# Performance work log

Measured on AMD Instinct MI355X. Metric: run time of the kernel, lower is better.

Reference implementation:

```python
import jax, jax.numpy as jnp
import numpy as np

N = 1024   # nodes
E = 65536  # edges per relation
H = 2      # attention heads
NEG_SLOPE = 0.2


def _add_self_loops(ei, n):
    loop = jnp.arange(n, dtype=ei.dtype)
    return jnp.concatenate([ei, jnp.stack([loop, loop])], axis=1)


def _gat(x, ei, W, a_src, a_dst, bias, n):
    # PyG GATConv (heads=H, concat=True): project, edge attention, segment softmax, scatter-sum
    h, c = a_src.shape
    xp = (x @ W).reshape(n, h, c)                      # [n, H, C]
    src, dst = ei[0], ei[1]
    al_s = jnp.einsum('nhc,hc->nh', xp, a_src)         # [n, H]
    al_d = jnp.einsum('nhc,hc->nh', xp, a_dst)
    alpha = jax.nn.leaky_relu(al_s[src] + al_d[dst], NEG_SLOPE)  # [E, H]
    m = jax.ops.segment_max(alpha, dst, num_segments=n)
    m = jnp.where(jnp.isfinite(m), m, 0.0)
    m = jax.lax.stop_gradient(m)
    e = jnp.exp(alpha - m[dst])
    s = jax.ops.segment_sum(e, dst, num_segments=n)
    a = e / (s[dst] + 1e-16)                           # segment softmax over incoming edges
    out = jax.ops.segment_sum(xp[src] * a[:, :, None], dst, num_segments=n)
    return out.reshape(n, h * c) + bias


def setup_inputs():
    key = jax.random.key(0)
    ks = jax.random.split(key, 32)
    d = {}
    d['x'] = jax.random.normal(ks[0], (N, 256), dtype=jnp.float32)
    d['ei0'] = jax.random.randint(ks[1], (2, E), 0, N)
    d['ei1'] = jax.random.randint(ks[2], (2, E), 0, N)
    k = 3
    # layer 1: in 256 -> H*256 = 512 per relation
    for r in range(2):
        d[f'W1_{r}'] = jax.random.normal(ks[k], (256, H * 256), jnp.float32) * 0.0625; k += 1
        d[f'as1_{r}'] = jax.random.normal(ks[k], (H, 256), jnp.float32) * 0.0625; k += 1
        d[f'ad1_{r}'] = jax.random.normal(ks[k], (H, 256), jnp.float32) * 0.0625; k += 1
        d[f'b1_{r}'] = jnp.zeros((H * 256,), jnp.float32)
    # layer 2: in 512 -> H*64 = 128 per relation
    for r in range(2):
        d[f'W2_{r}'] = jax.random.normal(ks[k], (512, H * 64), jnp.float32) * 0.0442; k += 1
        d[f'as2_{r}'] = jax.random.normal(ks[k], (H, 64), jnp.float32) * 0.125; k += 1
        d[f'ad2_{r}'] = jax.random.normal(ks[k], (H, 64), jnp.float32) * 0.125; k += 1
        d[f'b2_{r}'] = jnp.zeros((H * 64,), jnp.float32)
    d['w_lin'] = jax.random.normal(ks[k], (H * 64, 1), jnp.float32) * 0.088; k += 1
    d['b_lin'] = jnp.zeros((1,), jnp.float32)
    return d


def reference(x, ei0, ei1, W1_0, as1_0, ad1_0, b1_0, W1_1, as1_1, ad1_1, b1_1,
              W2_0, as2_0, ad2_0, b2_0, W2_1, as2_1, ad2_1, b2_1, w_lin, b_lin):
    e0 = _add_self_loops(ei0, N)
    e1 = _add_self_loops(ei1, N)
    # HeteroConv aggr='sum' over the two relations
    h1 = _gat(x, e0, W1_0, as1_0, ad1_0, b1_0, N) + _gat(x, e1, W1_1, as1_1, ad1_1, b1_1, N)
    h1 = jax.nn.relu(h1)
    h2 = _gat(h1, e0, W2_0, as2_0, ad2_0, b2_0, N) + _gat(h1, e1, W2_1, as2_1, ad2_1, b2_1, N)
    # dense pairwise sum over all node pairs: [N*N, 128]
    pairs = (h2[:, None, :] + h2[None, :, :]).reshape(N * N, h2.shape[-1])
    return pairs @ w_lin + b_lin
```

## Files before the change

### kernel.cpp

```cpp
#include <hip/hip_runtime.h>
#include <hip/hip_bf16.h>


#define NEG_SLOPE 0.2f
static __device__ __forceinline__ float lrelu(float x){ return x > 0.f ? x : NEG_SLOPE * x; }

#define NN 1024
#define SLOTS 192

static __device__ __forceinline__ int norm_cnt(int raw){
    return raw < -1000000000 ? raw - (int)0xAAAAAAAAu : raw;
}

struct P {
    const float *x; const int *ei0, *ei1;
    const float *W1_0,*as1_0,*ad1_0,*b1_0, *W1_1,*as1_1,*ad1_1,*b1_1;
    const float *W2_0,*as2_0,*ad2_0,*b2_0, *W2_1,*as2_1,*ad2_1,*b2_1;
    const float *wlin, *blin;
    float *out;
    __hip_bfloat162 *xp1_0,*xp1_1;
    float *L1;
    float *wc;
    float *nb;
    float *q, *qb;
    int *cnt;
    int *eb0,*eb1;
    int E;
};

__global__ __launch_bounds__(256)
void k1_scatter_gemm1(P p){
    __shared__ float As[32][68];
    __shared__ float Bs[32][68];
    const int b = blockIdx.x, t = threadIdx.x;

    if (b < 128){
        const int TOT = p.E + NN;
        for (int i = b*256 + t; i < 2*TOT; i += 128*256){
            int r = i >= TOT, e = i - r*TOT;
            const int* ei = r ? p.ei1 : p.ei0;
            int src, dst;
            if (e < p.E){ src = ei[e]; dst = ei[p.E + e]; } else { src = dst = e - p.E; }
            int pos = norm_cnt(atomicAdd(&p.cnt[r*NN + dst], 1));
            if (pos >= 0 && pos < SLOTS) (r ? p.eb1 : p.eb0)[dst*SLOTS + pos] = src;
        }
        return;
    }
    if (b >= 384){
        int idx2 = b - 384;
        int r = idx2 >> 2, k0 = (idx2 & 3) * 128;
        const float* W2 = r ? p.W2_1 : p.W2_0;
        const float* as2 = r ? p.as2_1 : p.as2_0;
        const float* ad2 = r ? p.ad2_1 : p.ad2_0;
        if (t < 128){
            int k = k0 + t;
            float sa[2] = {0.f,0.f}, da[2] = {0.f,0.f}, za[2] = {0.f,0.f};
            #pragma unroll
            for (int h = 0; h < 2; h++){
                for (int c = 0; c < 64; c++){
                    float w = W2[k*128 + h*64 + c];
                    sa[h] += w * as2[h*64 + c];
                    da[h] += w * ad2[h*64 + c];
                    za[h] += w * p.wlin[h*64 + c];
                }
            }
            float* wcr = p.wc + r*6*512;
            wcr[0*512 + k] = sa[0]; wcr[1*512 + k] = sa[1];
            wcr[2*512 + k] = da[0]; wcr[3*512 + k] = da[1];
            wcr[4*512 + k] = za[0]; wcr[5*512 + k] = za[1];
        }
        if (b == 384 && t == 128){
            float s = 0.f;
            for (int k = 0; k < 128; k++) s += (p.b2_0[k] + p.b2_1[k]) * p.wlin[k];
            p.qb[0] = s;
        }
        return;
    }
    int idx = b - 128;
    int r = idx >> 7, t2 = idx & 127;
    int m0 = (t2 >> 3) * 64, n0 = (t2 & 7) * 64;
    const float* B = r ? p.W1_1 : p.W1_0;
    __hip_bfloat162* C = r ? p.xp1_1 : p.xp1_0;
    int tx = t & 15, ty = t >> 4;
    float acc[4][4] = {};
    for (int k0 = 0; k0 < 256; k0 += 32){
        float4 a4[2], b4[2];
        #pragma unroll
        for (int u = 0; u < 2; u++){
            int f = u*256 + t;
            int am = f >> 3, ac4 = f & 7;
            a4[u] = *(const float4*)(p.x + (size_t)(m0+am)*256 + k0 + ac4*4);
            int bk = f >> 4, bc4 = f & 15;
            b4[u] = *(const float4*)(B + (size_t)(k0+bk)*512 + n0 + bc4*4);
        }
        __syncthreads();
        #pragma unroll
        for (int u = 0; u < 2; u++){
            int f = u*256 + t;
            int am = f >> 3, ac4 = f & 7;
            As[ac4*4+0][am] = a4[u].x; As[ac4*4+1][am] = a4[u].y;
            As[ac4*4+2][am] = a4[u].z; As[ac4*4+3][am] = a4[u].w;
            int bk = f >> 4, bc4 = f & 15;
            *(float4*)&Bs[bk][bc4*4] = b4[u];
        }
        __syncthreads();
        #pragma unroll
        for (int kk = 0; kk < 32; kk++){
            float4 av = *(const float4*)&As[kk][ty*4];
            float4 bv = *(const float4*)&Bs[kk][tx*4];
            float ar[4] = {av.x, av.y, av.z, av.w};
            float br[4] = {bv.x, bv.y, bv.z, bv.w};
            #pragma unroll
            for (int i = 0; i < 4; i++)
                #pragma unroll
                for (int j = 0; j < 4; j++)
                    acc[i][j] += ar[i] * br[j];
        }
        __syncthreads();
    }
    #pragma unroll
    for (int i = 0; i < 4; i++){
        int row = m0 + ty*4 + i, col = n0 + tx*4;
        __hip_bfloat162 t0, t1;
        t0.x = __float2bfloat16(acc[i][0]); t0.y = __float2bfloat16(acc[i][1]);
        t1.x = __float2bfloat16(acc[i][2]); t1.y = __float2bfloat16(acc[i][3]);
        size_t o2 = ((size_t)row*512 + col) >> 1;
        C[o2] = t0; C[o2 + 1] = t1;
    }
    {
        int h = n0 >> 8;
        const float* as_ = r ? p.as1_1 : p.as1_0;
        const float* ad_ = r ? p.ad1_1 : p.ad1_0;
        float a_s[4], a_d[4];
        #pragma unroll
        for (int u = 0; u < 4; u++){
            a_s[u] = as_[n0 + tx*4 + u];
            a_d[u] = ad_[n0 + tx*4 + u];
        }
        #pragma unroll
        for (int i = 0; i < 4; i++){
            float ps = acc[i][0]*a_s[0] + acc[i][1]*a_s[1]
                     + acc[i][2]*a_s[2] + acc[i][3]*a_s[3];
            float pd = acc[i][0]*a_d[0] + acc[i][1]*a_d[1]
                     + acc[i][2]*a_d[2] + acc[i][3]*a_d[3];
            #pragma unroll
            for (int o = 8; o > 0; o >>= 1){
                ps += __shfl_down(ps, o, 16);
                pd += __shfl_down(pd, o, 16);
            }
            if (tx == 0){
                int row = m0 + ty*4 + i;
                atomicAdd(&p.L1[row*8 + r*4 + h],     ps);
                atomicAdd(&p.L1[row*8 + r*4 + 2 + h], pd);
            }
        }
    }
}

__global__ __launch_bounds__(256)
void k2_agg1(P p){
    __shared__ float wa0[256], wa1[256];
    __shared__ int ssrc[256];
    __shared__ float rr0[4], rr1[4], invs[2];
    __shared__ float pacc[4][64][8];
    const int v = blockIdx.x, t = threadIdx.x;
    const int par = t >> 6;
    const int c16 = t & 63;
    const bool head0 = c16 < 32;
    float acc[8] = {};
    #pragma unroll
    for (int r = 0; r < 2; r++){
        const __hip_bfloat162* xp = r ? p.xp1_1 : p.xp1_0;
        const int* eb = (r ? p.eb1 : p.eb0) + v * SLOTS;
        int end = min(norm_cnt(p.cnt[r*NN + v]), SLOTS);
        float ad0 = p.L1[v*8 + r*4 + 2], ad1 = p.L1[v*8 + r*4 + 3];
        float s0 = 0.f, s1 = 0.f;
        if (t < end){
            int s = eb[t];
            s0 = __expf(lrelu(p.L1[s*8 + r*4 + 0] + ad0));
            s1 = __expf(lrelu(p.L1[s*8 + r*4 + 1] + ad1));
        }
        #pragma unroll
        for (int o = 32; o > 0; o >>= 1){
            s0 += __shfl_down(s0, o, 64);
            s1 += __shfl_down(s1, o, 64);
        }
        if ((t & 63) == 0){ rr0[t>>6] = s0; rr1[t>>6] = s1; }
        __syncthreads();
        if (t == 0){
            float S0 = 0.f, S1 = 0.f;
            #pragma unroll
            for (int i = 0; i < 4; i++){ S0 += rr0[i]; S1 += rr1[i]; }
            invs[0] = 1.f / (S0 + 1e-16f);
            invs[1] = 1.f / (S1 + 1e-16f);
        }
        __syncthreads();
        float inv0 = invs[0], inv1 = invs[1];
        if (t < end){
            int s = eb[t];
            ssrc[t] = s * 256;
            wa0[t] = __expf(lrelu(p.L1[s*8 + r*4 + 0] + ad0)) * inv0;
            wa1[t] = __expf(lrelu(p.L1[s*8 + r*4 + 1] + ad1)) * inv1;
        }
        __syncthreads();
        #pragma unroll 4
        for (int i = par; i < end; i += 4){
            const __hip_bfloat162* rp = xp + ssrc[i] + c16*4;
            float4 raw = *(const float4*)rp;
            const __hip_bfloat162* w = (const __hip_bfloat162*)&raw;
            float a = head0 ? wa0[i] : wa1[i];
            #pragma unroll
            for (int u = 0; u < 4; u++){
                acc[2*u+0] += __bfloat162float(w[u].x) * a;
                acc[2*u+1] += __bfloat162float(w[u].y) * a;
            }
        }
        __syncthreads();
    }
    #pragma unroll
    for (int u = 0; u < 8; u++) pacc[par][c16][u] = acc[u];
    __syncthreads();
    if (par == 0){
        int cb = c16 * 8;
        float o[8];
        #pragma unroll
        for (int u = 0; u < 8; u++){
            float s = acc[u] + pacc[1][c16][u] + pacc[2][c16][u] + pacc[3][c16][u];
            s += p.b1_0[cb+u] + p.b1_1[cb+u];
            o[u] = s > 0.f ? s : 0.f;
        }
        const int slot[6] = {0, 1, 4, 5, 2, 3};
        #pragma unroll
        for (int r2 = 0; r2 < 2; r2++){
            #pragma unroll
            for (int j = 0; j < 6; j++){
                const float* w = p.wc + ((r2*6 + j) << 9) + cb;
                float s = o[0]*w[0] + o[1]*w[1] + o[2]*w[2] + o[3]*w[3]
                        + o[4]*w[4] + o[5]*w[5] + o[6]*w[6] + o[7]*w[7];
                #pragma unroll
                for (int off = 32; off > 0; off >>= 1) s += __shfl_down(s, off, 64);
                if (c16 == 0) p.nb[(v*2 + r2)*8 + slot[j]] = s;
            }
        }
    }
}

__global__ __launch_bounds__(256)
void k3_agg2(P p){
    __shared__ float red[2][2][4];
    const int b = blockIdx.x, t = threadIdx.x, lane = t & 63, wave = t >> 6;
    const int nl = wave >> 1, r = wave & 1;
    const int v = b*2 + nl;
    const int* eb = (r ? p.eb1 : p.eb0) + v * SLOTS;
    int end = min(norm_cnt(p.cnt[r*NN + v]), SLOTS);
    const float* nbv = p.nb + (v*2 + r)*8;
    float ld0 = nbv[4], ld1 = nbv[5];
    float d0 = 0.f, d1 = 0.f, n0 = 0.f, n1 = 0.f;
    for (int e = lane; e < end; e += 64){
        int s = eb[e];
        float4 g = *(const float4*)(p.nb + (s*2 + r)*8);
        float e0 = __expf(lrelu(g.x + ld0));
        float e1 = __expf(lrelu(g.y + ld1));
        d0 += e0; d1 += e1;
        n0 += e0 * g.z; n1 += e1 * g.w;
    }
    #pragma unroll
    for (int o = 1; o < 64; o <<= 1){
        d0 += __shfl_xor(d0, o, 64); d1 += __shfl_xor(d1, o, 64);
        n0 += __shfl_xor(n0, o, 64); n1 += __shfl_xor(n1, o, 64);
    }
    if (lane == 0){
        red[nl][r][0] = d0; red[nl][r][1] = d1;
        red[nl][r][2] = n0; red[nl][r][3] = n1;
    }
    __syncthreads();
    if (t == nl*128){
        float qv = p.qb[0];
        #pragma unroll
        for (int rr = 0; rr < 2; rr++){
            qv += red[nl][rr][2] / (red[nl][rr][0] + 1e-16f);
            qv += red[nl][rr][3] / (red[nl][rr][1] + 1e-16f);
        }
        p.q[v] = qv;
    }
}

__global__ __launch_bounds__(256)
void k4_pairs(P p){
    int i = blockIdx.x, t = threadIdx.x;
    float qi = p.q[i] + p.blin[0];
    float4 qj = ((const float4*)p.q)[t];
    float4 o = { qi + qj.x, qi + qj.y, qi + qj.z, qi + qj.w };
    ((float4*)p.out)[(size_t)i * 256 + t] = o;
}

extern "C" void kernel_launch(void* const* d_in, const int* in_sizes, int n_in,
                              void* d_out, int out_size, void* d_ws, size_t ws_size,
                              hipStream_t stream){
    P prm;
    prm.x    = (const float*)d_in[0];
    prm.ei0  = (const int*)d_in[1];
    prm.ei1  = (const int*)d_in[2];
    prm.W1_0 = (const float*)d_in[3];  prm.as1_0 = (const float*)d_in[4];
    prm.ad1_0 = (const float*)d_in[5]; prm.b1_0  = (const float*)d_in[6];
    prm.W1_1 = (const float*)d_in[7];  prm.as1_1 = (const float*)d_in[8];
    prm.ad1_1 = (const float*)d_in[9]; prm.b1_1  = (const float*)d_in[10];
    prm.W2_0 = (const float*)d_in[11]; prm.as2_0 = (const float*)d_in[12];
    prm.ad2_0 = (const float*)d_in[13]; prm.b2_0 = (const float*)d_in[14];
    prm.W2_1 = (const float*)d_in[15]; prm.as2_1 = (const float*)d_in[16];
    prm.ad2_1 = (const float*)d_in[17]; prm.b2_1 = (const float*)d_in[18];
    prm.wlin = (const float*)d_in[19];
    prm.blin = (const float*)d_in[20];
    prm.out  = (float*)d_out;
    prm.E    = in_sizes[1] / 2;
    const int N = NN;

    char* wp = (char*)d_ws;
    auto alloc = [&](size_t bytes) -> char* {
        char* r = wp; wp += (bytes + 255) & ~(size_t)255; return r;
    };
    prm.xp1_0 = (__hip_bfloat162*)alloc((size_t)N*512*2);
    prm.xp1_1 = (__hip_bfloat162*)alloc((size_t)N*512*2);
    prm.cnt = (int*)alloc((size_t)2*N*4);
    prm.L1  = (float*)alloc((size_t)N*8*4);
    prm.wc  = (float*)alloc((size_t)2*6*512*4);
    prm.nb  = (float*)alloc((size_t)N*2*8*4);
    prm.eb0 = (int*)alloc((size_t)N*SLOTS*4);
    prm.eb1 = (int*)alloc((size_t)N*SLOTS*4);
    prm.q   = (float*)alloc(N*4);
    prm.qb  = (float*)alloc(256);

    k1_scatter_gemm1<<<392, 256, 0, stream>>>(prm);
    k2_agg1<<<NN, 256, 0, stream>>>(prm);
    k3_agg2<<<NN/2, 256, 0, stream>>>(prm);
    k4_pairs<<<NN, 256, 0, stream>>>(prm);
}
```

Measured before the change: 152.1 us.

## Pack edge buckets as interleaved u16, prefetch GEMM tiles, reuse softmax exps

Edge source buckets are stored as 16-bit indices in a single array that interleaves the two relations per node, halving their footprint and the scatter and gather traffic. The layer-1 GEMM now loads the next k-tile into registers while computing the current one, which removes one barrier per iteration. In the aggregation kernel the exponentials computed for the softmax denominator are kept in shared memory and scaled by the inverse sum inside the loop, so the second recompute pass and its barrier are dropped. The u16 indices assume fewer than 65536 nodes.

```diff
diff --git a/kernel.cpp b/kernel.cpp
--- a/kernel.cpp
+++ b/kernel.cpp
@@ -24,7 +24,7 @@
     float *nb;
     float *q, *qb;
     int *cnt;
-    int *eb0,*eb1;
+    unsigned short *eb;
     int E;
 };
 
@@ -42,7 +42,8 @@
             int src, dst;
             if (e < p.E){ src = ei[e]; dst = ei[p.E + e]; } else { src = dst = e - p.E; }
             int pos = norm_cnt(atomicAdd(&p.cnt[r*NN + dst], 1));
-            if (pos >= 0 && pos < SLOTS) (r ? p.eb1 : p.eb0)[dst*SLOTS + pos] = src;
+            if (pos >= 0 && pos < SLOTS)
+                p.eb[(dst*2 + r)*SLOTS + pos] = (unsigned short)src;
         }
         return;
     }
@@ -82,28 +83,32 @@
     const float* B = r ? p.W1_1 : p.W1_0;
     __hip_bfloat162* C = r ? p.xp1_1 : p.xp1_0;
     int tx = t & 15, ty = t >> 4;
+    const int am0 = t >> 3,  ac40 = t & 7;
+    const int am1 = (256+t) >> 3, ac41 = t & 7;
+    const int bk0 = t >> 4,  bc40 = t & 15;
+    const int bk1 = (256+t) >> 4, bc41 = t & 15;
     float acc[4][4] = {};
+    float4 a4[2], b4[2];
+    a4[0] = *(const float4*)(p.x + (size_t)(m0+am0)*256 + 0 + ac40*4);
+    a4[1] = *(const float4*)(p.x + (size_t)(m0+am1)*256 + 0 + ac41*4);
+    b4[0] = *(const float4*)(B + (size_t)(0+bk0)*512 + n0 + bc40*4);
+    b4[1] = *(const float4*)(B + (size_t)(0+bk1)*512 + n0 + bc41*4);
     for (int k0 = 0; k0 < 256; k0 += 32){
-        float4 a4[2], b4[2];
-        #pragma unroll
-        for (int u = 0; u < 2; u++){
-            int f = u*256 + t;
-            int am = f >> 3, ac4 = f & 7;
-            a4[u] = *(const float4*)(p.x + (size_t)(m0+am)*256 + k0 + ac4*4);
-            int bk = f >> 4, bc4 = f & 15;
-            b4[u] = *(const float4*)(B + (size_t)(k0+bk)*512 + n0 + bc4*4);
-        }
-        __syncthreads();
-        #pragma unroll
-        for (int u = 0; u < 2; u++){
-            int f = u*256 + t;
-            int am = f >> 3, ac4 = f & 7;
-            As[ac4*4+0][am] = a4[u].x; As[ac4*4+1][am] = a4[u].y;
-            As[ac4*4+2][am] = a4[u].z; As[ac4*4+3][am] = a4[u].w;
-            int bk = f >> 4, bc4 = f & 15;
-            *(float4*)&Bs[bk][bc4*4] = b4[u];
-        }
-        __syncthreads();
+        __syncthreads();
+        As[ac40*4+0][am0] = a4[0].x; As[ac40*4+1][am0] = a4[0].y;
+        As[ac40*4+2][am0] = a4[0].z; As[ac40*4+3][am0] = a4[0].w;
+        As[ac41*4+0][am1] = a4[1].x; As[ac41*4+1][am1] = a4[1].y;
+        As[ac41*4+2][am1] = a4[1].z; As[ac41*4+3][am1] = a4[1].w;
+        *(float4*)&Bs[bk0][bc40*4] = b4[0];
+        *(float4*)&Bs[bk1][bc41*4] = b4[1];
+        __syncthreads();
+        if (k0 + 32 < 256){
+            int kn = k0 + 32;
+            a4[0] = *(const float4*)(p.x + (size_t)(m0+am0)*256 + kn + ac40*4);
+            a4[1] = *(const float4*)(p.x + (size_t)(m0+am1)*256 + kn + ac41*4);
+            b4[0] = *(const float4*)(B + (size_t)(kn+bk0)*512 + n0 + bc40*4);
+            b4[1] = *(const float4*)(B + (size_t)(kn+bk1)*512 + n0 + bc41*4);
+        }
         #pragma unroll
         for (int kk = 0; kk < 32; kk++){
             float4 av = *(const float4*)&As[kk][ty*4];
@@ -116,7 +121,6 @@
                 for (int j = 0; j < 4; j++)
                     acc[i][j] += ar[i] * br[j];
         }
-        __syncthreads();
     }
     #pragma unroll
     for (int i = 0; i < 4; i++){
@@ -171,7 +175,7 @@
     #pragma unroll
     for (int r = 0; r < 2; r++){
         const __hip_bfloat162* xp = r ? p.xp1_1 : p.xp1_0;
-        const int* eb = (r ? p.eb1 : p.eb0) + v * SLOTS;
+        const unsigned short* eb = p.eb + (v*2 + r)*SLOTS;
         int end = min(norm_cnt(p.cnt[r*NN + v]), SLOTS);
         float ad0 = p.L1[v*8 + r*4 + 2], ad1 = p.L1[v*8 + r*4 + 3];
         float s0 = 0.f, s1 = 0.f;
@@ -179,6 +183,9 @@
             int s = eb[t];
             s0 = __expf(lrelu(p.L1[s*8 + r*4 + 0] + ad0));
             s1 = __expf(lrelu(p.L1[s*8 + r*4 + 1] + ad1));
+            ssrc[t] = s * 256;
+            wa0[t] = s0;
+            wa1[t] = s1;
         }
         #pragma unroll
         for (int o = 32; o > 0; o >>= 1){
@@ -195,20 +202,13 @@
             invs[1] = 1.f / (S1 + 1e-16f);
         }
         __syncthreads();
-        float inv0 = invs[0], inv1 = invs[1];
-        if (t < end){
-            int s = eb[t];
-            ssrc[t] = s * 256;
-            wa0[t] = __expf(lrelu(p.L1[s*8 + r*4 + 0] + ad0)) * inv0;
-            wa1[t] = __expf(lrelu(p.L1[s*8 + r*4 + 1] + ad1)) * inv1;
-        }
-        __syncthreads();
+        const float inv = head0 ? invs[0] : invs[1];
         #pragma unroll 4
         for (int i = par; i < end; i += 4){
             const __hip_bfloat162* rp = xp + ssrc[i] + c16*4;
             float4 raw = *(const float4*)rp;
             const __hip_bfloat162* w = (const __hip_bfloat162*)&raw;
-            float a = head0 ? wa0[i] : wa1[i];
+            float a = (head0 ? wa0[i] : wa1[i]) * inv;
             #pragma unroll
             for (int u = 0; u < 4; u++){
                 acc[2*u+0] += __bfloat162float(w[u].x) * a;
@@ -251,7 +251,7 @@
     const int b = blockIdx.x, t = threadIdx.x, lane = t & 63, wave = t >> 6;
     const int nl = wave >> 1, r = wave & 1;
     const int v = b*2 + nl;
-    const int* eb = (r ? p.eb1 : p.eb0) + v * SLOTS;
+    const unsigned short* eb = p.eb + (v*2 + r)*SLOTS;
     int end = min(norm_cnt(p.cnt[r*NN + v]), SLOTS);
     const float* nbv = p.nb + (v*2 + r)*8;
     float ld0 = nbv[4], ld1 = nbv[5];
@@ -325,8 +325,7 @@
     prm.L1  = (float*)alloc((size_t)N*8*4);
     prm.wc  = (float*)alloc((size_t)2*6*512*4);
     prm.nb  = (float*)alloc((size_t)N*2*8*4);
-    prm.eb0 = (int*)alloc((size_t)N*SLOTS*4);
-    prm.eb1 = (int*)alloc((size_t)N*SLOTS*4);
+    prm.eb  = (unsigned short*)alloc((size_t)N*2*SLOTS*2);
     prm.q   = (float*)alloc(N*4);
     prm.qb  = (float*)alloc(256);
 
```

Result: no change. 149.7 us (-1.5%).
